# Optimization experiments

Hardware: AMD Instinct MI355X
Metric: run time of the kernel (lower is better)

Reference implementation:

```python
import jax, jax.numpy as jnp
import numpy as np

B, N, HIDDEN = 4, 2048, 512
N_HEADS, HEAD_DIM = 8, 64
N_CANCER = 32
SCALE = float(np.sqrt(HEAD_DIM))


def setup_inputs() -> dict:
    key = jax.random.key(0)
    ks = jax.random.split(key, 16)
    s = 0.02
    return {
        "x": jax.random.normal(ks[0], (B, N, HIDDEN), dtype=jnp.float32),
        "cancer_type": jax.random.randint(ks[1], (B,), 0, N_CANCER, dtype=jnp.int64),
        "attn_mask": jnp.zeros((B, N), dtype=bool),
        "wq": jax.random.normal(ks[2], (HIDDEN, HIDDEN), dtype=jnp.float32) * s,
        "bq": jnp.zeros((HIDDEN,), dtype=jnp.float32),
        "wk": jax.random.normal(ks[3], (HIDDEN, HIDDEN), dtype=jnp.float32) * s,
        "bk": jnp.zeros((HIDDEN,), dtype=jnp.float32),
        "wv": jax.random.normal(ks[4], (HIDDEN, HIDDEN), dtype=jnp.float32) * s,
        "bv": jnp.zeros((HIDDEN,), dtype=jnp.float32),
        "wo": jax.random.normal(ks[5], (HIDDEN, HIDDEN), dtype=jnp.float32) * s,
        "bo": jnp.zeros((HIDDEN,), dtype=jnp.float32),
        "bias_emb": jax.random.normal(ks[6], (N_CANCER, N_HEADS), dtype=jnp.float32) * s,
        "keymod_emb": jax.random.normal(ks[7], (N_CANCER, HIDDEN), dtype=jnp.float32) * s,
    }


def reference(x, cancer_type, attn_mask, wq, bq, wk, bk, wv, bv, wo, bo, bias_emb, keymod_emb):
    Bc, Nc, _ = x.shape
    # projections (torch Linear: x @ W.T + b), split heads -> (B, H, N, D)
    def split_heads(t):
        return t.reshape(Bc, Nc, N_HEADS, HEAD_DIM).transpose(0, 2, 1, 3)
    q = split_heads(x @ wq.T + bq)
    k = split_heads(x @ wk.T + bk)
    v = split_heads(x @ wv.T + bv)
    # cancer-conditioned key offset: (B, H, 1, D)
    ct_key = keymod_emb[cancer_type].reshape(Bc, 1, N_HEADS, HEAD_DIM).transpose(0, 2, 1, 3)
    k = k + ct_key
    # scores + per-head cancer bias
    attn = jnp.einsum("bhnd,bhmd->bhnm", q, k) / SCALE
    ct_bias = bias_emb[cancer_type]  # (B, H)
    attn = attn + ct_bias[:, :, None, None]
    attn = jnp.where(attn_mask[:, None, None, :], -jnp.inf, attn)
    attn = jax.nn.softmax(attn, axis=-1)
    # dropout is identity in eval mode
    out = jnp.einsum("bhnm,bhmd->bhnd", attn, v)
    out = out.transpose(0, 2, 1, 3).reshape(Bc, Nc, HIDDEN)
    return out @ wo.T + bo
```

## Files before the change

### kernel.cpp

```cpp
#include <hip/hip_runtime.h>

#define B_    4
#define N_    2048
#define HID   512
#define NH    8
#define HD    64
#define TOK   (B_ * N_)
#define LOG2E 1.4426950408889634f

typedef __attribute__((ext_vector_type(8))) short short8;
typedef __attribute__((ext_vector_type(4))) float f32x4;
typedef unsigned short u16;

static __device__ __forceinline__ u16 f2bf(float f) {
    unsigned int u = __builtin_bit_cast(unsigned int, f);
    u += 0x7FFFu + ((u >> 16) & 1u);
    return (u16)(u >> 16);
}
static __device__ __forceinline__ unsigned pktrunc(float a, float b) {
    return __builtin_amdgcn_perm(__builtin_bit_cast(unsigned, b),
                                 __builtin_bit_cast(unsigned, a), 0x07060302u);
}

static __device__ __forceinline__ void dma16(const void* g, void* l) {
    __builtin_amdgcn_global_load_lds(
        (const __attribute__((address_space(1))) unsigned int*)(unsigned long long)g,
        (__attribute__((address_space(3))) unsigned int*)(unsigned int)(unsigned long long)l,
        16, 0, 0);
}

__global__ __launch_bounds__(256) void cvt_all(
    const float* __restrict__ x,
    const float* __restrict__ w0, const float* __restrict__ w1,
    const float* __restrict__ w2, const float* __restrict__ w3,
    u16* __restrict__ xb,
    u16* __restrict__ d0, u16* __restrict__ d1,
    u16* __restrict__ d2, u16* __restrict__ d3)
{
    const int bid = blockIdx.x;
    const float* s;
    u16* d;
    int off;
    if (bid < 4096) { s = x; d = xb; off = bid; }
    else {
        const int t = (bid - 4096) >> 8;
        off = (bid - 4096) & 255;
        s = t == 0 ? w0 : t == 1 ? w1 : t == 2 ? w2 : w3;
        d = t == 0 ? d0 : t == 1 ? d1 : t == 2 ? d2 : d3;
    }
    const int i = off * 1024 + threadIdx.x * 4;
    const float4 v = *(const float4*)&s[i];
    ushort4 o;
    o.x = f2bf(v.x); o.y = f2bf(v.y); o.z = f2bf(v.z); o.w = f2bf(v.w);
    *(ushort4*)&d[i] = o;
}

__global__ __launch_bounds__(256) void gemm_mfma(
    const u16* __restrict__ A,
    const u16* __restrict__ W0, const u16* __restrict__ W1, const u16* __restrict__ W2,
    const float* __restrict__ bias0, const float* __restrict__ bias1, const float* __restrict__ bias2,
    void* __restrict__ C0, void* __restrict__ C1, void* __restrict__ C2,
    int qkv)
{
    const int z = blockIdx.z;
    const u16*   W    = z == 0 ? W0 : z == 1 ? W1 : W2;
    const float* bias = z == 0 ? bias0 : z == 1 ? bias1 : bias2;

    __shared__ u16 ABs[2][2][128 * 32];

    const int tid  = threadIdx.x;
    const int row0 = blockIdx.x * 128, col0 = blockIdx.y * 128;
    const int w    = tid >> 6, lane = tid & 63;
    const int wr   = w >> 1, wc = w & 1;
    const int t16  = lane & 15, q4 = lane >> 4;

    const int dmr  = lane >> 2;
    const int dmc8 = (lane & 3) ^ ((lane >> 2) & 3) ^ ((lane >> 4) & 3);

    f32x4 acc[4][4];
    #pragma unroll
    for (int mt = 0; mt < 4; ++mt)
        #pragma unroll
        for (int nt = 0; nt < 4; ++nt)
            acc[mt][nt] = (f32x4){0.f, 0.f, 0.f, 0.f};

    #define GEMM_DMA(p, k0)                                                     \
        _Pragma("unroll")                                                       \
        for (int i = 0; i < 2; ++i) {                                           \
            const int c = w * 2 + i;                                            \
            dma16(&A[(size_t)(row0 + c * 16 + dmr) * HID + (k0) + dmc8 * 8],    \
                  &ABs[p][0][c * 512]);                                         \
            dma16(&W[(size_t)(col0 + c * 16 + dmr) * HID + (k0) + dmc8 * 8],    \
                  &ABs[p][1][c * 512]);                                         \
        }

    GEMM_DMA(0, 0)

    const int swz = (t16 ^ (t16 >> 2)) & 3;

    for (int it = 0; it < HID / 32; ++it) {
        __syncthreads();
        if (it + 1 < HID / 32) { GEMM_DMA((it + 1) & 1, (it + 1) * 32) }

        const int p = it & 1;
        short8 af[4], bf[4];
        #pragma unroll
        for (int mt = 0; mt < 4; ++mt)
            af[mt] = *(const short8*)&ABs[p][0][(wr * 64 + mt * 16 + t16) * 32 + (q4 ^ swz) * 8];
        #pragma unroll
        for (int nt = 0; nt < 4; ++nt)
            bf[nt] = *(const short8*)&ABs[p][1][(wc * 64 + nt * 16 + t16) * 32 + (q4 ^ swz) * 8];
        #pragma unroll
        for (int mt = 0; mt < 4; ++mt)
            #pragma unroll
            for (int nt = 0; nt < 4; ++nt)
                acc[mt][nt] = __builtin_amdgcn_mfma_f32_16x16x32_bf16(
                    af[mt], bf[nt], acc[mt][nt], 0, 0, 0);
    }

    if (!qkv) {
        #pragma unroll
        for (int nt = 0; nt < 4; ++nt) {
            const int j = col0 + wc * 64 + nt * 16 + t16;
            const float bv = bias[j];
            #pragma unroll
            for (int mt = 0; mt < 4; ++mt)
                #pragma unroll
                for (int r = 0; r < 4; ++r) {
                    const int i = row0 + wr * 64 + mt * 16 + q4 * 4 + r;
                    ((float*)C0)[(size_t)i * HID + j] = acc[mt][nt][r] + bv;
                }
        }
    } else if (z < 2) {
        const float qscale = (z == 0) ? 0.125f * LOG2E : 1.0f;
        u16* C = (u16*)(z == 0 ? C0 : C1);
        #pragma unroll
        for (int nt = 0; nt < 4; ++nt) {
            const int j = col0 + wc * 64 + nt * 16 + t16;
            const float bv = bias[j];
            const int h = j >> 6, d = j & 63;
            #pragma unroll
            for (int mt = 0; mt < 4; ++mt)
                #pragma unroll
                for (int r = 0; r < 4; ++r) {
                    const int i = row0 + wr * 64 + mt * 16 + q4 * 4 + r;
                    const int b = i >> 11, n = i & (N_ - 1);
                    C[(((size_t)(b * NH + h)) * N_ + n) * HD + d] =
                        f2bf((acc[mt][nt][r] + bv) * qscale);
                }
        }
    } else {
        u16* Vt = (u16*)C2;
        u16 (*St)[72] = (u16(*)[72])&ABs[0][0][0];
        const int b = row0 >> 11;
        #pragma unroll
        for (int p = 0; p < 2; ++p) {
            __syncthreads();
            if (wr == p) {
                #pragma unroll
                for (int nt = 0; nt < 4; ++nt) {
                    const int jp = wc * 64 + nt * 16 + t16;
                    const float bv = bias[col0 + jp];
                    #pragma unroll
                    for (int mt = 0; mt < 4; ++mt) {
                        uint2 pk;
                        pk.x = pktrunc(acc[mt][nt][0] + bv, acc[mt][nt][1] + bv);
                        pk.y = pktrunc(acc[mt][nt][2] + bv, acc[mt][nt][3] + bv);
                        *(uint2*)&St[jp][mt * 16 + q4 * 4] = pk;
                    }
                }
            }
            __syncthreads();
            const int nb = (row0 & (N_ - 1)) + p * 64;
            #pragma unroll
            for (int it = 0; it < 2; ++it) {
                const int task = tid + it * 256;
                const int jp = task >> 2, qc = task & 3;
                u16 v[16];
                #pragma unroll
                for (int e = 0; e < 16; ++e) {
                    const int np = qc * 16 + e;
                    const int n  = ((np & 3) << 4) | (np >> 2);
                    v[e] = St[jp][n];
                }
                const int j = col0 + jp, h = j >> 6, d = j & 63;
                u16* dst = &Vt[(((size_t)(b * NH + h)) * HD + d) * N_ + nb + qc * 16];
                *(short8*)(dst)     = *(const short8*)&v[0];
                *(short8*)(dst + 8) = *(const short8*)&v[8];
            }
        }
    }
}

__global__ __launch_bounds__(256) void flash_mfma(
    const u16* __restrict__ Qg, const u16* __restrict__ Kg,
    const u16* __restrict__ Vtg, const unsigned char* __restrict__ msk,
    u16* __restrict__ AOg)
{
    __shared__ u16 KVs[2][2][64 * 64];
    __shared__ u16 Ps[4][32][72];
    __shared__ unsigned Mnd[N_ / 64][32];

    const int tid = threadIdx.x;
    const int w = tid >> 6, lane = tid & 63;
    const int t16 = lane & 15, q4 = lane >> 4;
    const int bh = blockIdx.y, b = bh >> 3, h = bh & 7;
    const int qrow0 = blockIdx.x * 128;
    const int qbase = qrow0 + w * 32;

    const size_t hb = (size_t)bh * N_ * HD;
    const u16* Qh  = Qg + hb;
    const u16* Kh  = Kg + hb;
    const u16* Vth = Vtg + hb;
    const unsigned char* mrow = msk + b * N_;

    #pragma unroll
    for (int it = 0; it < 4; ++it) {
        const int e = tid + it * 256;
        const int kt = e >> 5, sl = e & 31;
        const int tt = sl >> 1, wd = sl & 1;
        const int k0 = kt * 64 + wd * 32 + tt;
        const unsigned lo = mrow[k0]      ? 0u : 0x0000FFFFu;
        const unsigned hi = mrow[k0 + 16] ? 0u : 0xFFFF0000u;
        Mnd[kt][sl] = lo | hi;
    }

    short8 qf[2][2];
    #pragma unroll
    for (int mt = 0; mt < 2; ++mt)
        #pragma unroll
        for (int kk = 0; kk < 2; ++kk)
            qf[mt][kk] = *(const short8*)
                &Qh[(size_t)(qbase + mt * 16 + t16) * HD + kk * 32 + q4 * 8];

    const short8 ones8 = {0x3F80, 0x3F80, 0x3F80, 0x3F80,
                          0x3F80, 0x3F80, 0x3F80, 0x3F80};

    f32x4 o[2][4], ls[2];
    #pragma unroll
    for (int mt = 0; mt < 2; ++mt) {
        #pragma unroll
        for (int nt = 0; nt < 4; ++nt) o[mt][nt] = (f32x4){0.f, 0.f, 0.f, 0.f};
        ls[mt] = (f32x4){0.f, 0.f, 0.f, 0.f};
    }

    const int dmr  = lane >> 3;
    const int dmc8 = (lane & 7) ^ ((lane >> 3) & 7);

    #define FLASH_DMA(p, kb)                                                    \
        _Pragma("unroll")                                                       \
        for (int i = 0; i < 2; ++i) {                                           \
            const int c = w * 2 + i;                                            \
            dma16(&Kh[(size_t)((kb) + c * 8 + dmr) * HD + dmc8 * 8],            \
                  &KVs[p][0][c * 512]);                                         \
            dma16(&Vth[(size_t)(c * 8 + dmr) * N_ + (kb) + dmc8 * 8],           \
                  &KVs[p][1][c * 512]);                                         \
        }

    FLASH_DMA(0, 0)

    const int swz7 = t16 & 7;

    for (int kt = 0; kt < N_ / 64; ++kt) {
        __syncthreads();
        if (kt + 1 < N_ / 64) { FLASH_DMA((kt + 1) & 1, (kt + 1) * 64) }
        const int p = kt & 1;

        f32x4 s[2][4];
        #pragma unroll
        for (int mt = 0; mt < 2; ++mt)
            #pragma unroll
            for (int f = 0; f < 4; ++f)
                s[mt][f] = (f32x4){0.f, 0.f, 0.f, 0.f};
        #pragma unroll
        for (int f = 0; f < 4; ++f) {
            #pragma unroll
            for (int kk = 0; kk < 2; ++kk) {
                const short8 kf = *(const short8*)
                    &KVs[p][0][(f * 16 + t16) * 64 + ((kk * 4 + q4) ^ swz7) * 8];
                #pragma unroll
                for (int mt = 0; mt < 2; ++mt)
                    s[mt][f] = __builtin_amdgcn_mfma_f32_16x16x32_bf16(
                        qf[mt][kk], kf, s[mt][f], 0, 0, 0);
            }
        }

        const uint2 mnd = *(const uint2*)&Mnd[kt][t16 * 2];

        #pragma unroll
        for (int mt = 0; mt < 2; ++mt) {
            #pragma unroll
            for (int r = 0; r < 4; ++r) {
                const float e0 = __builtin_amdgcn_exp2f(s[mt][0][r]);
                const float e1 = __builtin_amdgcn_exp2f(s[mt][1][r]);
                const float e2 = __builtin_amdgcn_exp2f(s[mt][2][r]);
                const float e3 = __builtin_amdgcn_exp2f(s[mt][3][r]);
                uint2 pk;
                pk.x = pktrunc(e0, e1) & mnd.x;
                pk.y = pktrunc(e2, e3) & mnd.y;
                *(uint2*)&Ps[w][mt * 16 + q4 * 4 + r][t16 * 4] = pk;
            }
        }

        short8 pf[2][2];
        #pragma unroll
        for (int mt = 0; mt < 2; ++mt)
            #pragma unroll
            for (int kk = 0; kk < 2; ++kk)
                pf[mt][kk] = *(const short8*)&Ps[w][mt * 16 + t16][kk * 32 + q4 * 8];
        #pragma unroll
        for (int mt = 0; mt < 2; ++mt)
            #pragma unroll
            for (int kk = 0; kk < 2; ++kk)
                ls[mt] = __builtin_amdgcn_mfma_f32_16x16x32_bf16(
                    pf[mt][kk], ones8, ls[mt], 0, 0, 0);
        #pragma unroll
        for (int nt = 0; nt < 4; ++nt) {
            #pragma unroll
            for (int kk = 0; kk < 2; ++kk) {
                const short8 vf = *(const short8*)
                    &KVs[p][1][(nt * 16 + t16) * 64 + ((kk * 4 + q4) ^ swz7) * 8];
                #pragma unroll
                for (int mt = 0; mt < 2; ++mt)
                    o[mt][nt] = __builtin_amdgcn_mfma_f32_16x16x32_bf16(
                        pf[mt][kk], vf, o[mt][nt], 0, 0, 0);
            }
        }
    }

    #pragma unroll
    for (int mt = 0; mt < 2; ++mt) {
        #pragma unroll
        for (int r = 0; r < 4; ++r) {
            const float inv = 1.f / ls[mt][r];
            const int n = qbase + mt * 16 + q4 * 4 + r;
            #pragma unroll
            for (int nt = 0; nt < 4; ++nt)
                AOg[((size_t)(b * N_ + n)) * HID + h * 64 + nt * 16 + t16] =
                    f2bf(o[mt][nt][r] * inv);
        }
    }
}

extern "C" void kernel_launch(void* const* d_in, const int* in_sizes, int n_in,
                              void* d_out, int out_size, void* d_ws, size_t ws_size,
                              hipStream_t stream) {
    const float* x  = (const float*)d_in[0];
    const unsigned char* mask = (const unsigned char*)d_in[2];
    const float* wq = (const float*)d_in[3];
    const float* bq = (const float*)d_in[4];
    const float* wk = (const float*)d_in[5];
    const float* bk = (const float*)d_in[6];
    const float* wv = (const float*)d_in[7];
    const float* bv = (const float*)d_in[8];
    const float* wo = (const float*)d_in[9];
    const float* bo = (const float*)d_in[10];

    char* ws = (char*)d_ws;
    u16* xb  = (u16*)(ws);
    u16* wqb = (u16*)(ws + (8u << 20));
    u16* wkb = (u16*)(ws + (8u << 20) + (512u << 10));
    u16* wvb = (u16*)(ws + (8u << 20) + (1024u << 10));
    u16* wob = (u16*)(ws + (8u << 20) + (1536u << 10));
    u16* Qg  = (u16*)(ws + (10u << 20));
    u16* Kg  = (u16*)(ws + (18u << 20));
    u16* Vtg = (u16*)(ws + (26u << 20));
    u16* AOg = xb;

    cvt_all<<<5120, 256, 0, stream>>>(x, wq, wk, wv, wo, xb, wqb, wkb, wvb, wob);

    gemm_mfma<<<dim3(TOK / 128, HID / 128, 3), 256, 0, stream>>>(
        xb, wqb, wkb, wvb, bq, bk, bv, Qg, Kg, Vtg, 1);

    flash_mfma<<<dim3(N_ / 128, B_ * NH), 256, 0, stream>>>(Qg, Kg, Vtg, mask, AOg);

    gemm_mfma<<<dim3(TOK / 128, HID / 128, 1), 256, 0, stream>>>(
        AOg, wob, wob, wob, bo, bo, bo, d_out, d_out, d_out, 0);
}
```

Measured before the change: 178.8 us.

## Split attention over key halves, coalesce QKV stores, and retile output GEMM

The attention kernel gets a second grid dimension that splits the key range in two. Each half writes unnormalized partial outputs in bf16 plus row sums, and a new reduce kernel adds the halves and normalizes them into the attention-output buffer. The Q/K projection is computed transposed and staged through LDS so that head-major stores are written as coalesced 16-byte chunks. The output projection becomes its own kernel with 64-row tiles, which doubles the block count. Together these aim for more parallelism and cheaper stores, at the cost of an extra launch, an extra round trip through global memory, and some precision loss from storing the partials in bf16.

```diff
diff --git a/kernel.cpp b/kernel.cpp
--- a/kernel.cpp
+++ b/kernel.cpp
@@ -16,6 +16,9 @@
     unsigned int u = __builtin_bit_cast(unsigned int, f);
     u += 0x7FFFu + ((u >> 16) & 1u);
     return (u16)(u >> 16);
+}
+static __device__ __forceinline__ float bf2f(u16 v) {
+    return __builtin_bit_cast(float, (unsigned)v << 16);
 }
 static __device__ __forceinline__ unsigned pktrunc(float a, float b) {
     return __builtin_amdgcn_perm(__builtin_bit_cast(unsigned, b),
@@ -55,21 +58,23 @@
     *(ushort4*)&d[i] = o;
 }
 
-__global__ __launch_bounds__(256) void gemm_mfma(
-    const u16* __restrict__ A,
+__global__ __launch_bounds__(256) void gemm_qkv(
+    const u16* __restrict__ xb,
     const u16* __restrict__ W0, const u16* __restrict__ W1, const u16* __restrict__ W2,
     const float* __restrict__ bias0, const float* __restrict__ bias1, const float* __restrict__ bias2,
-    void* __restrict__ C0, void* __restrict__ C1, void* __restrict__ C2,
-    int qkv)
+    u16* __restrict__ Qg, u16* __restrict__ Kg, u16* __restrict__ Vtg)
 {
     const int z = blockIdx.z;
-    const u16*   W    = z == 0 ? W0 : z == 1 ? W1 : W2;
+    const u16*   Wz   = z == 0 ? W0 : z == 1 ? W1 : W2;
     const float* bias = z == 0 ? bias0 : z == 1 ? bias1 : bias2;
 
+    const u16* Ap; const u16* Bp; int arow0, brow0;
+    if (z < 2) { Ap = Wz; Bp = xb; arow0 = blockIdx.y * 128; brow0 = blockIdx.x * 128; }
+    else       { Ap = xb; Bp = Wz; arow0 = blockIdx.x * 128; brow0 = blockIdx.y * 128; }
+
     __shared__ u16 ABs[2][2][128 * 32];
 
     const int tid  = threadIdx.x;
-    const int row0 = blockIdx.x * 128, col0 = blockIdx.y * 128;
     const int w    = tid >> 6, lane = tid & 63;
     const int wr   = w >> 1, wc = w & 1;
     const int t16  = lane & 15, q4 = lane >> 4;
@@ -84,23 +89,23 @@
         for (int nt = 0; nt < 4; ++nt)
             acc[mt][nt] = (f32x4){0.f, 0.f, 0.f, 0.f};
 
-    #define GEMM_DMA(p, k0)                                                     \
+    #define QKV_DMA(p, k0)                                                      \
         _Pragma("unroll")                                                       \
         for (int i = 0; i < 2; ++i) {                                           \
             const int c = w * 2 + i;                                            \
-            dma16(&A[(size_t)(row0 + c * 16 + dmr) * HID + (k0) + dmc8 * 8],    \
+            dma16(&Ap[(size_t)(arow0 + c * 16 + dmr) * HID + (k0) + dmc8 * 8],  \
                   &ABs[p][0][c * 512]);                                         \
-            dma16(&W[(size_t)(col0 + c * 16 + dmr) * HID + (k0) + dmc8 * 8],    \
+            dma16(&Bp[(size_t)(brow0 + c * 16 + dmr) * HID + (k0) + dmc8 * 8],  \
                   &ABs[p][1][c * 512]);                                         \
         }
 
-    GEMM_DMA(0, 0)
+    QKV_DMA(0, 0)
 
     const int swz = (t16 ^ (t16 >> 2)) & 3;
 
     for (int it = 0; it < HID / 32; ++it) {
         __syncthreads();
-        if (it + 1 < HID / 32) { GEMM_DMA((it + 1) & 1, (it + 1) * 32) }
+        if (it + 1 < HID / 32) { QKV_DMA((it + 1) & 1, (it + 1) * 32) }
 
         const int p = it & 1;
         short8 af[4], bf[4];
@@ -118,41 +123,44 @@
                     af[mt], bf[nt], acc[mt][nt], 0, 0, 0);
     }
 
-    if (!qkv) {
-        #pragma unroll
-        for (int nt = 0; nt < 4; ++nt) {
-            const int j = col0 + wc * 64 + nt * 16 + t16;
-            const float bv = bias[j];
-            #pragma unroll
-            for (int mt = 0; mt < 4; ++mt)
+    if (z < 2) {
+        const float qs = (z == 0) ? 0.125f * LOG2E : 1.0f;
+        u16* Cg = (z == 0) ? Qg : Kg;
+        u16 (*St)[72] = (u16(*)[72])&ABs[0][0][0];
+        #pragma unroll
+        for (int p = 0; p < 2; ++p) {
+            __syncthreads();
+            if (wr == p) {
                 #pragma unroll
-                for (int r = 0; r < 4; ++r) {
-                    const int i = row0 + wr * 64 + mt * 16 + q4 * 4 + r;
-                    ((float*)C0)[(size_t)i * HID + j] = acc[mt][nt][r] + bv;
+                for (int mt = 0; mt < 4; ++mt) {
+                    const f32x4 bv = *(const f32x4*)&bias[arow0 + p * 64 + mt * 16 + q4 * 4];
+                    #pragma unroll
+                    for (int nt = 0; nt < 4; ++nt) {
+                        const int np = wc * 64 + nt * 16 + t16;
+                        uint2 pk;
+                        pk.x = pktrunc((acc[mt][nt][0] + bv[0]) * qs,
+                                       (acc[mt][nt][1] + bv[1]) * qs);
+                        pk.y = pktrunc((acc[mt][nt][2] + bv[2]) * qs,
+                                       (acc[mt][nt][3] + bv[3]) * qs);
+                        *(uint2*)&St[np][mt * 16 + q4 * 4] = pk;
+                    }
                 }
-        }
-    } else if (z < 2) {
-        const float qscale = (z == 0) ? 0.125f * LOG2E : 1.0f;
-        u16* C = (u16*)(z == 0 ? C0 : C1);
-        #pragma unroll
-        for (int nt = 0; nt < 4; ++nt) {
-            const int j = col0 + wc * 64 + nt * 16 + t16;
-            const float bv = bias[j];
-            const int h = j >> 6, d = j & 63;
-            #pragma unroll
-            for (int mt = 0; mt < 4; ++mt)
-                #pragma unroll
-                for (int r = 0; r < 4; ++r) {
-                    const int i = row0 + wr * 64 + mt * 16 + q4 * 4 + r;
-                    const int b = i >> 11, n = i & (N_ - 1);
-                    C[(((size_t)(b * NH + h)) * N_ + n) * HD + d] =
-                        f2bf((acc[mt][nt][r] + bv) * qscale);
-                }
+            }
+            __syncthreads();
+            const int h = blockIdx.y * 2 + p;
+            #pragma unroll
+            for (int it = 0; it < 4; ++it) {
+                const int task = tid + it * 256;
+                const int np = task >> 3, ch = task & 7;
+                const int nf = brow0 + np;
+                const int b = nf >> 11, n = nf & (N_ - 1);
+                *(short8*)&Cg[(((size_t)(b * NH + h)) * N_ + n) * HD + ch * 8] =
+                    *(const short8*)&St[np][ch * 8];
+            }
         }
     } else {
-        u16* Vt = (u16*)C2;
         u16 (*St)[72] = (u16(*)[72])&ABs[0][0][0];
-        const int b = row0 >> 11;
+        const int b = arow0 >> 11;
         #pragma unroll
         for (int p = 0; p < 2; ++p) {
             __syncthreads();
@@ -160,7 +168,7 @@
                 #pragma unroll
                 for (int nt = 0; nt < 4; ++nt) {
                     const int jp = wc * 64 + nt * 16 + t16;
-                    const float bv = bias[col0 + jp];
+                    const float bv = bias[brow0 + jp];
                     #pragma unroll
                     for (int mt = 0; mt < 4; ++mt) {
                         uint2 pk;
@@ -171,7 +179,7 @@
                 }
             }
             __syncthreads();
-            const int nb = (row0 & (N_ - 1)) + p * 64;
+            const int nb = (arow0 & (N_ - 1)) + p * 64;
             #pragma unroll
             for (int it = 0; it < 2; ++it) {
                 const int task = tid + it * 256;
@@ -183,28 +191,100 @@
                     const int n  = ((np & 3) << 4) | (np >> 2);
                     v[e] = St[jp][n];
                 }
-                const int j = col0 + jp, h = j >> 6, d = j & 63;
-                u16* dst = &Vt[(((size_t)(b * NH + h)) * HD + d) * N_ + nb + qc * 16];
+                const int j = brow0 + jp, h = j >> 6, d = j & 63;
+                u16* dst = &Vtg[(((size_t)(b * NH + h)) * HD + d) * N_ + nb + qc * 16];
                 *(short8*)(dst)     = *(const short8*)&v[0];
                 *(short8*)(dst + 8) = *(const short8*)&v[8];
             }
         }
+    }
+}
+
+__global__ __launch_bounds__(256) void gemm_o(
+    const u16* __restrict__ A, const u16* __restrict__ W,
+    const float* __restrict__ bias, float* __restrict__ C)
+{
+    __shared__ u16 ABs[2][(64 + 128) * 32];
+
+    const int tid  = threadIdx.x;
+    const int row0 = blockIdx.x * 64, col0 = blockIdx.y * 128;
+    const int w    = tid >> 6, lane = tid & 63;
+    const int wr   = w >> 1, wc = w & 1;
+    const int t16  = lane & 15, q4 = lane >> 4;
+
+    const int dmr  = lane >> 2;
+    const int dmc8 = (lane & 3) ^ ((lane >> 2) & 3) ^ ((lane >> 4) & 3);
+
+    f32x4 acc[2][4];
+    #pragma unroll
+    for (int mt = 0; mt < 2; ++mt)
+        #pragma unroll
+        for (int nt = 0; nt < 4; ++nt)
+            acc[mt][nt] = (f32x4){0.f, 0.f, 0.f, 0.f};
+
+    #define O_DMA(p, k0)                                                        \
+        dma16(&A[(size_t)(row0 + w * 16 + dmr) * HID + (k0) + dmc8 * 8],        \
+              &ABs[p][w * 512]);                                                \
+        _Pragma("unroll")                                                       \
+        for (int i = 0; i < 2; ++i) {                                           \
+            const int c = w * 2 + i;                                            \
+            dma16(&W[(size_t)(col0 + c * 16 + dmr) * HID + (k0) + dmc8 * 8],    \
+                  &ABs[p][2048 + c * 512]);                                     \
+        }
+
+    O_DMA(0, 0)
+
+    const int swz = (t16 ^ (t16 >> 2)) & 3;
+
+    for (int it = 0; it < HID / 32; ++it) {
+        __syncthreads();
+        if (it + 1 < HID / 32) { O_DMA((it + 1) & 1, (it + 1) * 32) }
+
+        const int p = it & 1;
+        short8 af[2], bf[4];
+        #pragma unroll
+        for (int mt = 0; mt < 2; ++mt)
+            af[mt] = *(const short8*)&ABs[p][(wr * 32 + mt * 16 + t16) * 32 + (q4 ^ swz) * 8];
+        #pragma unroll
+        for (int nt = 0; nt < 4; ++nt)
+            bf[nt] = *(const short8*)&ABs[p][2048 + (wc * 64 + nt * 16 + t16) * 32 + (q4 ^ swz) * 8];
+        #pragma unroll
+        for (int mt = 0; mt < 2; ++mt)
+            #pragma unroll
+            for (int nt = 0; nt < 4; ++nt)
+                acc[mt][nt] = __builtin_amdgcn_mfma_f32_16x16x32_bf16(
+                    af[mt], bf[nt], acc[mt][nt], 0, 0, 0);
+    }
+
+    #pragma unroll
+    for (int nt = 0; nt < 4; ++nt) {
+        const int j = col0 + wc * 64 + nt * 16 + t16;
+        const float bv = bias[j];
+        #pragma unroll
+        for (int mt = 0; mt < 2; ++mt)
+            #pragma unroll
+            for (int r = 0; r < 4; ++r) {
+                const int i = row0 + wr * 32 + mt * 16 + q4 * 4 + r;
+                C[(size_t)i * HID + j] = acc[mt][nt][r] + bv;
+            }
     }
 }
 
 __global__ __launch_bounds__(256) void flash_mfma(
     const u16* __restrict__ Qg, const u16* __restrict__ Kg,
     const u16* __restrict__ Vtg, const unsigned char* __restrict__ msk,
-    u16* __restrict__ AOg)
+    u16* __restrict__ Op, float* __restrict__ Lp)
 {
     __shared__ u16 KVs[2][2][64 * 64];
     __shared__ u16 Ps[4][32][72];
-    __shared__ unsigned Mnd[N_ / 64][32];
+    __shared__ unsigned Mnd[16][32];
 
     const int tid = threadIdx.x;
     const int w = tid >> 6, lane = tid & 63;
     const int t16 = lane & 15, q4 = lane >> 4;
-    const int bh = blockIdx.y, b = bh >> 3, h = bh & 7;
+    const int bh = blockIdx.y, b = bh >> 3;
+    const int z = blockIdx.z;
+    const int kofs = z * (N_ / 2);
     const int qrow0 = blockIdx.x * 128;
     const int qbase = qrow0 + w * 32;
 
@@ -215,11 +295,11 @@
     const unsigned char* mrow = msk + b * N_;
 
     #pragma unroll
-    for (int it = 0; it < 4; ++it) {
+    for (int it = 0; it < 2; ++it) {
         const int e = tid + it * 256;
         const int kt = e >> 5, sl = e & 31;
         const int tt = sl >> 1, wd = sl & 1;
-        const int k0 = kt * 64 + wd * 32 + tt;
+        const int k0 = kofs + kt * 64 + wd * 32 + tt;
         const unsigned lo = mrow[k0]      ? 0u : 0x0000FFFFu;
         const unsigned hi = mrow[k0 + 16] ? 0u : 0xFFFF0000u;
         Mnd[kt][sl] = lo | hi;
@@ -257,13 +337,13 @@
                   &KVs[p][1][c * 512]);                                         \
         }
 
-    FLASH_DMA(0, 0)
+    FLASH_DMA(0, kofs)
 
     const int swz7 = t16 & 7;
 
-    for (int kt = 0; kt < N_ / 64; ++kt) {
+    for (int kt = 0; kt < 16; ++kt) {
         __syncthreads();
-        if (kt + 1 < N_ / 64) { FLASH_DMA((kt + 1) & 1, (kt + 1) * 64) }
+        if (kt + 1 < 16) { FLASH_DMA((kt + 1) & 1, kofs + (kt + 1) * 64) }
         const int p = kt & 1;
 
         f32x4 s[2][4];
@@ -328,18 +408,39 @@
         }
     }
 
+    const size_t obase = (((size_t)z * 32 + bh)) * N_ * HD;
     #pragma unroll
     for (int mt = 0; mt < 2; ++mt) {
         #pragma unroll
         for (int r = 0; r < 4; ++r) {
-            const float inv = 1.f / ls[mt][r];
             const int n = qbase + mt * 16 + q4 * 4 + r;
+            if (t16 == 0) Lp[((size_t)z * 32 + bh) * N_ + n] = ls[mt][r];
             #pragma unroll
             for (int nt = 0; nt < 4; ++nt)
-                AOg[((size_t)(b * N_ + n)) * HID + h * 64 + nt * 16 + t16] =
-                    f2bf(o[mt][nt][r] * inv);
-        }
-    }
+                Op[obase + (size_t)n * HD + nt * 16 + t16] = f2bf(o[mt][nt][r]);
+        }
+    }
+}
+
+__global__ __launch_bounds__(256) void reduce_o(
+    const u16* __restrict__ Op, const float* __restrict__ Lp,
+    u16* __restrict__ AOg)
+{
+    const int e = blockIdx.x * 256 + threadIdx.x;
+    const int d4 = e & 15;
+    const int n  = (e >> 4) & (N_ - 1);
+    const int bh = e >> 15;
+    const size_t base = (((size_t)bh) * N_ + n) * HD + d4 * 4;
+    const ushort4 a = *(const ushort4*)&Op[base];
+    const ushort4 c = *(const ushort4*)&Op[(size_t)32 * N_ * HD + base];
+    const float inv = 1.f / (Lp[(size_t)bh * N_ + n] + Lp[(size_t)(32 + bh) * N_ + n]);
+    ushort4 o;
+    o.x = f2bf((bf2f(a.x) + bf2f(c.x)) * inv);
+    o.y = f2bf((bf2f(a.y) + bf2f(c.y)) * inv);
+    o.z = f2bf((bf2f(a.z) + bf2f(c.z)) * inv);
+    o.w = f2bf((bf2f(a.w) + bf2f(c.w)) * inv);
+    const int b = bh >> 3, h = bh & 7;
+    *(ushort4*)&AOg[(((size_t)b * N_ + n)) * HID + h * 64 + d4 * 4] = o;
 }
 
 extern "C" void kernel_launch(void* const* d_in, const int* in_sizes, int n_in,
@@ -365,15 +466,20 @@
     u16* Qg  = (u16*)(ws + (10u << 20));
     u16* Kg  = (u16*)(ws + (18u << 20));
     u16* Vtg = (u16*)(ws + (26u << 20));
+    u16* Op  = (u16*)(ws + (34u << 20));
+    float* Lp = (float*)(ws + (50u << 20));
     u16* AOg = xb;
 
     cvt_all<<<5120, 256, 0, stream>>>(x, wq, wk, wv, wo, xb, wqb, wkb, wvb, wob);
 
-    gemm_mfma<<<dim3(TOK / 128, HID / 128, 3), 256, 0, stream>>>(
-        xb, wqb, wkb, wvb, bq, bk, bv, Qg, Kg, Vtg, 1);
-
-    flash_mfma<<<dim3(N_ / 128, B_ * NH), 256, 0, stream>>>(Qg, Kg, Vtg, mask, AOg);
-
-    gemm_mfma<<<dim3(TOK / 128, HID / 128, 1), 256, 0, stream>>>(
-        AOg, wob, wob, wob, bo, bo, bo, d_out, d_out, d_out, 0);
-}
+    gemm_qkv<<<dim3(TOK / 128, HID / 128, 3), 256, 0, stream>>>(
+        xb, wqb, wkb, wvb, bq, bk, bv, Qg, Kg, Vtg);
+
+    flash_mfma<<<dim3(N_ / 128, B_ * NH, 2), 256, 0, stream>>>(
+        Qg, Kg, Vtg, mask, Op, Lp);
+
+    reduce_o<<<(32 * N_ * 16) / 256, 256, 0, stream>>>(Op, Lp, AOg);
+
+    gemm_o<<<dim3(TOK / 64, HID / 128), 256, 0, stream>>>(
+        AOg, wob, bo, (float*)d_out);
+}
```

Measured after the change: 179.3 us. Within noise of the previous version (+0.3%).
